# Kernel optimization log

Hardware: AMD Instinct MI355X
Metric: run time of the kernel (lower is better)

Reference implementation:

```python
import jax, jax.numpy as jnp
import numpy as np

CELL = 8
POS_MARGIN = 1.0
NEG_MARGIN = 0.2
LAMBDA_D = 250.0
LAMBDA_LOSS = 0.0001


def _resize_bilinear(x, out_h, out_w):
    # torch F.interpolate(..., mode='bilinear', align_corners=False) half-pixel sampling
    B, H, W = x.shape
    def axis(n_in, n_out):
        src = (jnp.arange(n_out, dtype=jnp.float32) + 0.5) * (n_in / n_out) - 0.5
        src = jnp.clip(src, 0.0, n_in - 1.0)
        i0 = jnp.floor(src).astype(jnp.int32)
        i1 = jnp.minimum(i0 + 1, n_in - 1)
        w = src - i0.astype(jnp.float32)
        return i0, i1, w
    r0, r1, wr = axis(H, out_h)
    xr = x[:, r0, :] * (1.0 - wr)[None, :, None] + x[:, r1, :] * wr[None, :, None]
    c0, c1, wc = axis(W, out_w)
    return xr[:, :, c0] * (1.0 - wc)[None, None, :] + xr[:, :, c1] * wc[None, None, :]


def detector_loss(pred, heatmap, vm):
    eps = 1e-7
    pos_inds = (heatmap == 1.0).astype(pred.dtype)
    neg_inds = (heatmap < 1.0).astype(pred.dtype)
    neg_weights = (1.0 - heatmap) ** 4
    num_pos = pos_inds.sum()
    pos_loss = (jnp.log(pred + eps) * (1.0 - pred) ** 2 * pos_inds * vm).sum()
    neg_loss = (jnp.log(1.0 - pred + eps) * pred ** 2 * neg_weights * neg_inds * vm).sum()
    return jnp.where(num_pos == 0, -neg_loss, -(pos_loss + neg_loss) / jnp.maximum(num_pos, 1.0))


def descriptor_loss(desc, wdesc, Hmat, vm, wvm):
    B, D, Hc, Wc = desc.shape
    N = Hc * Wc
    # cell-center coordinates in (row=y, col=x) order
    ii, jj = np.meshgrid(np.arange(Hc), np.arange(Wc), indexing='ij')
    coords = (np.stack([ii, jj], axis=-1) * CELL + CELL // 2).astype(np.float32)  # [Hc,Wc,2]
    coords = jnp.asarray(coords)
    pts = coords.reshape(-1, 2)
    # warp points with homographies (convert (y,x) -> (x,y), apply H, convert back)
    H_list = Hmat[:, 0]  # [B,3,3]
    homog = jnp.concatenate([pts[:, ::-1], jnp.ones((N, 1), jnp.float32)], axis=-1)  # [N,3]
    w = jnp.einsum('bij,nj->bni', H_list, homog)
    warped = (w[..., :2] / w[..., 2:3])[..., ::-1]  # back to (y,x), [B,N,2]
    warped = warped.reshape(B, Hc, Wc, 1, 1, 2)
    cell_dist = jnp.linalg.norm(coords.reshape(1, 1, 1, Hc, Wc, 2) - warped, axis=-1)  # [B,Hc,Wc,Hc,Wc]
    s = (cell_dist <= CELL - 0.5).astype(jnp.float32)

    normalization = wvm.sum()
    vm_c = _resize_bilinear(vm, Hc, Wc) > 0.5
    wvm_c = _resize_bilinear(wvm, Hc, Wc) > 0.5
    valid_pair = (vm_c.reshape(B, Hc, Wc, 1, 1) & wvm_c.reshape(B, 1, 1, Hc, Wc)).astype(jnp.float32)

    def l2norm(x):
        return x / jnp.maximum(jnp.linalg.norm(x, axis=-1, keepdims=True), 1e-12)

    d = l2norm(jnp.transpose(desc, (0, 2, 3, 1)))    # [B,Hc,Wc,D]
    wd = l2norm(jnp.transpose(wdesc, (0, 2, 3, 1)))  # [B,Hc,Wc,D]
    dot = jnp.einsum('bijd,bkld->bijkl', d, wd)      # all-pairs cosine sim
    dot = jax.nn.relu(dot)
    positive_dist = jnp.maximum(0.0, POS_MARGIN - dot)
    negative_dist = jnp.maximum(0.0, dot - NEG_MARGIN)
    loss = (LAMBDA_D * s * positive_dist + (1.0 - s) * negative_dist) * valid_pair
    return loss.sum() / normalization


def setup_inputs() -> dict:
    key = jax.random.key(0)
    ks = jax.random.split(key, 8)
    B, H, W, D, Hc, Wc = 2, 480, 640, 256, 60, 80
    Hmat = jnp.eye(3, dtype=jnp.float32)[None, None] + 0.05 * jax.random.normal(ks[6], (B, 1, 3, 3), jnp.float32)
    return {
        'prob': jax.random.uniform(ks[0], (B, H, W), jnp.float32),
        'ht': jax.random.uniform(ks[1], (B, H, W), jnp.float32),
        'valid_mask': jnp.ones((B, H, W), jnp.float32),
        'warped_prob': jax.random.uniform(ks[2], (B, H, W), jnp.float32),
        'warped_ht': jax.random.uniform(ks[3], (B, H, W), jnp.float32),
        'warped_valid_mask': jnp.ones((B, H, W), jnp.float32),
        'desc_raw': jax.random.normal(ks[4], (B, D, Hc, Wc), jnp.float32),
        'warped_desc_raw': jax.random.normal(ks[5], (B, D, Hc, Wc), jnp.float32),
        'Hmat': Hmat,
    }


def reference(prob, ht, valid_mask, warped_prob, warped_ht, warped_valid_mask, desc_raw, warped_desc_raw, Hmat):
    points_loss = detector_loss(prob, ht, valid_mask)
    warped_points_loss = detector_loss(warped_prob, warped_ht, warped_valid_mask)
    desc_loss = descriptor_loss(desc_raw, warped_desc_raw, Hmat, valid_mask, warped_valid_mask)
    total = points_loss + warped_points_loss + LAMBDA_LOSS * desc_loss
    return total, points_loss, warped_points_loss, desc_loss
```

## Files before the change

### kernel.cpp

```cpp
#include <hip/hip_runtime.h>
#include <hip/hip_bf16.h>
#include <cmath>

#define BB 2
#define HH 480
#define WW 640
#define DD 256
#define HC 60
#define WC 80
#define NN (HC*WC)

#define DET_BLOCKS 300
#define SUMSQ_NB ((NN + 255)/256)
#define P0_BLOCKS (2*DET_BLOCKS + 16*SUMSQ_NB)

#define NTILES64 (NN/64)
#define DESC_BLOCKS_F32 (BB*NTILES64*NTILES64)
#define TS3 96
#define BK 32
#define NT96 (NN/TS3)
#define BLK96 (NT96*NT96)
#define GEMM_BLOCKS (BB*BLK96)
#define CORR_BLOCKS (BB*NN/4)
#define DESC_GRID (GEMM_BLOCKS + CORR_BLOCKS)

#define OFF_DET0  0
#define OFF_DET1  2048
#define OFF_INVA  16384
#define OFF_INVB  (OFF_INVA + BB*NN)
#define OFF_WRW   (OFF_INVB + BB*NN)
#define OFF_WCL   (OFF_WRW + BB*NN)
#define OFF_VMC   (OFF_WCL + BB*NN)
#define OFF_WVMC  (OFF_VMC + BB*NN)
#define OFF_SQP   (OFF_WVMC + BB*NN)
#define OFF_DESCP (OFF_SQP + 16*NN)
#define OFF_TA    172032
#define TA_FLOATS (BB*NN*DD/2)
#define OFF_TB    (OFF_TA + TA_FLOATS)
#define WS_NEED   ((size_t)(OFF_TB + TA_FLOATS) * 4)

typedef __attribute__((ext_vector_type(8))) short short8;
typedef __attribute__((ext_vector_type(4))) float f32x4;

__device__ inline float bf2f(unsigned short u)
{
    unsigned int x = ((unsigned int)u) << 16;
    return __builtin_bit_cast(float, x);
}

__device__ inline void det_accum(float p, float h, float v,
                                 float& posl, float& negl, float& npos, float& vsum)
{
    float omp = 1.f - p;
    if (h == 1.0f) {
        posl += logf(p + 1e-7f) * omp*omp * v;
        npos += 1.f;
    }
    if (h < 1.0f) {
        float oh = 1.f - h;
        float w4 = oh*oh; w4 *= w4;
        negl += logf(omp + 1e-7f) * p*p * w4 * v;
    }
    vsum += v;
}

__global__ __launch_bounds__(256) void det_sumsq_kernel(
    const float* __restrict__ pred0, const float* __restrict__ hmap0, const float* __restrict__ vm0,
    const float* __restrict__ pred1, const float* __restrict__ hmap1, const float* __restrict__ vm1,
    const float* __restrict__ desc, const float* __restrict__ wdesc,
    float* __restrict__ ws)
{
    const int bidx = blockIdx.x;
    if (bidx >= 2*DET_BLOCKS) {
        const int sid   = bidx - 2*DET_BLOCKS;
        const int combo = sid / SUMSQ_NB;
        const int nb    = sid % SUMSQ_NB;
        const int z  = combo >> 2;
        const int dc = combo & 3;
        const int n  = nb*256 + threadIdx.x;
        if (n >= NN) return;
        const float* src = ((z & 1) ? wdesc : desc) + (size_t)(z >> 1)*DD*NN;
        float s = 0.f;
        const int d0 = dc*64;
        #pragma unroll 8
        for (int d = d0; d < d0 + 64; ++d) {
            float v = src[(size_t)d*NN + n];
            s = fmaf(v, v, s);
        }
        ws[OFF_SQP + ((size_t)z*4 + dc)*NN + n] = s;
        return;
    }
    const int set = bidx / DET_BLOCKS;
    const int db  = bidx % DET_BLOCKS;
    const float4* pred = (const float4*)(set ? pred1 : pred0);
    const float4* hmap = (const float4*)(set ? hmap1 : hmap0);
    const float4* vm   = (const float4*)(set ? vm1   : vm0);
    float* partials = ws + (set ? OFF_DET1 : OFF_DET0);

    float posl = 0.f, negl = 0.f, npos = 0.f, vsum = 0.f;
    const int total4 = BB*HH*WW/4;
    for (int i = db*256 + threadIdx.x; i < total4; i += DET_BLOCKS*256) {
        float4 p = pred[i], h = hmap[i], v = vm[i];
        det_accum(p.x, h.x, v.x, posl, negl, npos, vsum);
        det_accum(p.y, h.y, v.y, posl, negl, npos, vsum);
        det_accum(p.z, h.z, v.z, posl, negl, npos, vsum);
        det_accum(p.w, h.w, v.w, posl, negl, npos, vsum);
    }
    __shared__ float red[256];
    int t = threadIdx.x;
    float vals[4] = {posl, negl, npos, vsum};
    for (int j = 0; j < 4; ++j) {
        red[t] = vals[j]; __syncthreads();
        for (int s = 128; s > 0; s >>= 1) { if (t < s) red[t] += red[t+s]; __syncthreads(); }
        if (t == 0) partials[db*4 + j] = red[0];
        __syncthreads();
    }
}

__device__ inline float bilin_cell(const float* __restrict__ x, int i, int j)
{
    float sr = (i + 0.5f) * ((float)HH/(float)HC) - 0.5f;
    sr = fminf(fmaxf(sr, 0.f), (float)(HH-1));
    int r0 = (int)floorf(sr); int r1 = min(r0+1, HH-1); float wr = sr - (float)r0;
    float sc = (j + 0.5f) * ((float)WW/(float)WC) - 0.5f;
    sc = fminf(fmaxf(sc, 0.f), (float)(WW-1));
    int c0 = (int)floorf(sc); int c1 = min(c0+1, WW-1); float wc = sc - (float)c0;
    float v00 = x[r0*WW+c0], v01 = x[r0*WW+c1];
    float v10 = x[r1*WW+c0], v11 = x[r1*WW+c1];
    float e0 = v00*(1.f-wr) + v10*wr;
    float e1 = v01*(1.f-wr) + v11*wr;
    return e0*(1.f-wc) + e1*wc;
}

__device__ inline void prep_geom(int idx, const float* __restrict__ vm,
                                 const float* __restrict__ wvm,
                                 const float* __restrict__ Hmat, float* __restrict__ ws)
{
    int b = idx / NN, n = idx % NN;
    int i = n / WC, j = n % WC;
    float px = (float)(j*8 + 4), py = (float)(i*8 + 4);
    const float* Hb = Hmat + b*9;
    float w0 = Hb[0]*px + Hb[1]*py + Hb[2];
    float w1 = Hb[3]*px + Hb[4]*py + Hb[5];
    float w2 = Hb[6]*px + Hb[7]*py + Hb[8];
    ws[OFF_WRW + idx] = w1 / w2;
    ws[OFF_WCL + idx] = w0 / w2;
    ws[OFF_VMC  + idx] = (bilin_cell(vm  + (size_t)b*HH*WW, i, j) > 0.5f) ? 1.f : 0.f;
    ws[OFF_WVMC + idx] = (bilin_cell(wvm + (size_t)b*HH*WW, i, j) > 0.5f) ? 1.f : 0.f;
}

__global__ __launch_bounds__(256) void prep_kernel(
    const float* __restrict__ vm, const float* __restrict__ wvm,
    const float* __restrict__ Hmat, float* __restrict__ ws)
{
    int idx = blockIdx.x*256 + threadIdx.x;
    if (idx >= BB*NN) return;
    int b = idx / NN, n = idx % NN;

    const float* sq = ws + OFF_SQP;
    float sa = 0.f, sb = 0.f;
    #pragma unroll
    for (int k = 0; k < 4; ++k) {
        sa += sq[((b*2+0)*4 + k)*NN + n];
        sb += sq[((b*2+1)*4 + k)*NN + n];
    }
    ws[OFF_INVA + idx] = 1.f / fmaxf(sqrtf(sa), 1e-12f);
    ws[OFF_INVB + idx] = 1.f / fmaxf(sqrtf(sb), 1e-12f);
    prep_geom(idx, vm, wvm, Hmat, ws);
}

__global__ __launch_bounds__(256) void prep_kernel_full(
    const float* __restrict__ desc, const float* __restrict__ wdesc,
    const float* __restrict__ vm, const float* __restrict__ wvm,
    const float* __restrict__ Hmat, float* __restrict__ ws)
{
    int idx = blockIdx.x*256 + threadIdx.x;
    if (idx >= BB*NN) return;
    int b = idx / NN, n = idx % NN;

    const float* a  = desc  + (size_t)b*DD*NN + n;
    const float* bp = wdesc + (size_t)b*DD*NN + n;
    float sa = 0.f, sb = 0.f;
    for (int d = 0; d < DD; ++d) {
        float x = a[(size_t)d*NN];  sa = fmaf(x, x, sa);
        float y = bp[(size_t)d*NN]; sb = fmaf(y, y, sb);
    }
    ws[OFF_INVA + idx] = 1.f / fmaxf(sqrtf(sa), 1e-12f);
    ws[OFF_INVB + idx] = 1.f / fmaxf(sqrtf(sb), 1e-12f);
    prep_geom(idx, vm, wvm, Hmat, ws);
}

__global__ __launch_bounds__(256) void transpose_kernel(
    const float* __restrict__ desc, const float* __restrict__ wdesc,
    unsigned short* __restrict__ ta, unsigned short* __restrict__ tb,
    const float* __restrict__ ws)
{
    const int nb = blockIdx.x * 64;
    const int db = blockIdx.y * 64;
    const int z  = blockIdx.z;
    const int b  = z >> 1;
    const float* src = (z & 1) ? wdesc : desc;
    unsigned short* dst = (z & 1) ? tb : ta;
    src += (size_t)b*DD*NN;
    dst += (size_t)b*NN*DD;

    __shared__ float tile[64][65];
    const int tr = threadIdx.x >> 6;
    const int tc = threadIdx.x & 63;
    #pragma unroll
    for (int i = 0; i < 16; ++i) {
        int d = db + i*4 + tr;
        tile[i*4 + tr][tc] = src[(size_t)d*NN + nb + tc];
    }
    __syncthreads();
    const int idxn = b*NN + nb + tc;
    const float scl = (z & 1) ? ws[OFF_INVB + idxn] * ws[OFF_WVMC + idxn]
                              : ws[OFF_INVA + idxn] * ws[OFF_VMC  + idxn];
    #pragma unroll
    for (int gg = 0; gg < 2; ++gg) {
        int g = tr + gg*4;
        short8 v8;
        #pragma unroll
        for (int j = 0; j < 8; ++j) {
            float v = tile[g*8 + j][tc] * scl;
            __hip_bfloat16 h = __float2bfloat16(v);
            v8[j] = (short)__builtin_bit_cast(unsigned short, h);
        }
        int sg = (db >> 3) + g;
        *(short8*)(dst + ((size_t)sg*NN + nb + tc)*8) = v8;
    }
}

__global__ __launch_bounds__(256) void desc_mfma(
    const unsigned short* __restrict__ ta, const unsigned short* __restrict__ tb,
    const float* __restrict__ ws, float* __restrict__ partials)
{
    __shared__ unsigned short As[3][TS3*BK];
    __shared__ unsigned short Bs[3][TS3*BK];
    __shared__ float corr_red[4];

    const int bidx = blockIdx.x;
    const int tid  = threadIdx.x;
    const int lane = tid & 63;
    const int wid  = tid >> 6;

    if (bidx < CORR_BLOCKS) {
        const int idx = bidx*4 + wid;
        const int cb  = idx / NN, cn = idx % NN;
        const float wrow = ws[OFF_WRW + idx];
        const float wcol = ws[OFF_WCL + idx];
        const float va   = ws[OFF_VMC + idx];
        const unsigned short* tA = ta + (size_t)cb*NN*DD;
        const unsigned short* tB = tb + (size_t)cb*NN*DD;
        const float* wvmc = ws + OFF_WVMC + cb*NN;

        const int sg = lane >> 1;
        const int e  = (lane & 1) * 4;
        const unsigned short* ap = tA + ((size_t)sg*NN + cn)*8 + e;
        float a0 = bf2f(ap[0]), a1 = bf2f(ap[1]), a2 = bf2f(ap[2]), a3 = bf2f(ap[3]);

        const int ibase = (int)floorf((wrow - 4.f) * 0.125f);
        const int jbase = (int)floorf((wcol - 4.f) * 0.125f);
        float corr = 0.f;
        #pragma unroll
        for (int di = 0; di < 2; ++di) {
            #pragma unroll
            for (int dj = 0; dj < 2; ++dj) {
                int ii = ibase + di, jj = jbase + dj;
                float dr = (float)(ii*8 + 4) - wrow;
                float dc = (float)(jj*8 + 4) - wcol;
                bool ok = (ii >= 0) && (ii < HC) && (jj >= 0) && (jj < WC)
                          && (dr*dr + dc*dc) <= 56.25f;
                if (ok) {
                    int m = ii*WC + jj;
                    const unsigned short* bp = tB + ((size_t)sg*NN + m)*8 + e;
                    float d = a0*bf2f(bp[0]);
                    d = fmaf(a1, bf2f(bp[1]), d);
                    d = fmaf(a2, bf2f(bp[2]), d);
                    d = fmaf(a3, bf2f(bp[3]), d);
                    #pragma unroll
                    for (int off = 1; off < 64; off <<= 1)
                        d += __shfl_xor(d, off, 64);
                    float dotr = fmaxf(d, 0.f);
                    float pos = 250.f * fmaxf(1.f - dotr, 0.f);
                    float neg = fmaxf(d - 0.2f, 0.f);
                    corr += (pos - neg) * va * wvmc[m];
                }
            }
        }
        if (lane == 0) corr_red[wid] = corr;
        __syncthreads();
        if (tid == 0)
            partials[bidx] = corr_red[0] + corr_red[1] + corr_red[2] + corr_red[3];
        return;
    }

    const int g   = bidx - CORR_BLOCKS;
    const int swz = (g & 7) * (GEMM_BLOCKS/8) + (g >> 3);
    const int b   = swz / BLK96;
    const int rr  = swz % BLK96;
    const int n0  = (rr / NT96) * TS3;
    const int m0  = (rr % NT96) * TS3;

    const unsigned short* tab = ta + (size_t)b*NN*DD;
    const unsigned short* tbb = tb + (size_t)b*NN*DD;

#define STAGE(t_, buf_)                                                          \
    {                                                                            \
        _Pragma("unroll")                                                        \
        for (int c = 0; c < 3; ++c) {                                            \
            int c2 = wid*3 + c;                                                  \
            int cA = (c2 < 6) ? c2 : (c2 - 6);                                   \
            int o  = cA*64 + lane;                                               \
            int s  = o / TS3;                                                    \
            int r  = o - s*TS3;                                                  \
            const unsigned short* gp = (c2 < 6)                                  \
                ? (tab + ((size_t)((t_)*4 + s)*NN + n0 + r)*8)                   \
                : (tbb + ((size_t)((t_)*4 + s)*NN + m0 + r)*8);                  \
            unsigned short* l0 = (c2 < 6) ? &As[buf_][cA*512] : &Bs[buf_][cA*512];\
            __builtin_amdgcn_global_load_lds(                                    \
                (const __attribute__((address_space(1))) void*)gp,               \
                (__attribute__((address_space(3))) void*)l0, 16, 0, 0);          \
        }                                                                        \
    }

    const int wr = wid >> 1, wc = wid & 1;
    const int ln15   = lane & 15;
    const int slot16 = lane >> 4;
    f32x4 acc[3][3] = {};

    STAGE(0, 0);
    STAGE(1, 1);

    #pragma unroll
    for (int t = 0; t < 8; ++t) {
        if (t < 7) asm volatile("s_waitcnt vmcnt(3)" ::: "memory");
        else       asm volatile("s_waitcnt vmcnt(0)" ::: "memory");
        __builtin_amdgcn_s_barrier();
        __builtin_amdgcn_sched_barrier(0);
        const unsigned short* Ab = As[t % 3];
        const unsigned short* Bb = Bs[t % 3];
        short8 af[3], bf[3];
        #pragma unroll
        for (int f = 0; f < 3; ++f) {
            int ra = wr*48 + f*16 + ln15;
            af[f] = *(const short8*)(Ab + (slot16*TS3 + ra)*8);
            int rb = wc*48 + f*16 + ln15;
            bf[f] = *(const short8*)(Bb + (slot16*TS3 + rb)*8);
        }
        if (t < 6) STAGE(t+2, (t+2) % 3);
        #pragma unroll
        for (int fi = 0; fi < 3; ++fi)
            #pragma unroll
            for (int fj = 0; fj < 3; ++fj)
                acc[fi][fj] = __builtin_amdgcn_mfma_f32_16x16x32_bf16(
                    af[fi], bf[fj], acc[fi][fj], 0, 0, 0);
    }

    float sum = 0.f;
    #pragma unroll
    for (int fi = 0; fi < 3; ++fi)
        #pragma unroll
        for (int fj = 0; fj < 3; ++fj)
            #pragma unroll
            for (int reg = 0; reg < 4; ++reg)
                sum += fmaxf(acc[fi][fj][reg] - 0.2f, 0.f);

    float* red = (float*)&As[0][0];
    red[tid] = sum; __syncthreads();
    for (int s = 128; s > 0; s >>= 1) { if (tid < s) red[tid] += red[tid+s]; __syncthreads(); }
    if (tid == 0) partials[bidx] = red[0];
#undef STAGE
}

__global__ __launch_bounds__(256) void desc_kernel(
    const float* __restrict__ desc, const float* __restrict__ wdesc,
    const float* __restrict__ ws, float* __restrict__ partials)
{
    const int b  = blockIdx.z;
    const int n0 = blockIdx.y * 64;
    const int m0 = blockIdx.x * 64;
    const float* A  = desc  + (size_t)b*DD*NN;
    const float* Bm = wdesc + (size_t)b*DD*NN;

    __shared__ float As[32][64];
    __shared__ float Bs[32][64];

    const int tid = threadIdx.x;
    const int tx = tid & 15, ty = tid >> 4;
    float acc[4][4] = {{0.f}};

    for (int k0 = 0; k0 < DD; k0 += 32) {
        #pragma unroll
        for (int l = 0; l < 8; ++l) {
            int e = tid + l*256;
            int kk = e >> 6, nn = e & 63;
            As[kk][nn] = A [(size_t)(k0+kk)*NN + n0 + nn];
            Bs[kk][nn] = Bm[(size_t)(k0+kk)*NN + m0 + nn];
        }
        __syncthreads();
        #pragma unroll
        for (int kk = 0; kk < 32; ++kk) {
            float4 av = *reinterpret_cast<const float4*>(&As[kk][ty*4]);
            float4 bv = *reinterpret_cast<const float4*>(&Bs[kk][tx*4]);
            float a4[4] = {av.x, av.y, av.z, av.w};
            float b4[4] = {bv.x, bv.y, bv.z, bv.w};
            #pragma unroll
            for (int r = 0; r < 4; ++r)
                #pragma unroll
                for (int c = 0; c < 4; ++c)
                    acc[r][c] = fmaf(a4[r], b4[c], acc[r][c]);
        }
        __syncthreads();
    }

    const float* inva = ws + OFF_INVA + b*NN;
    const float* invb = ws + OFF_INVB + b*NN;
    const float* wrp  = ws + OFF_WRW + b*NN;
    const float* wcp  = ws + OFF_WCL + b*NN;
    const float* vmc  = ws + OFF_VMC + b*NN;
    const float* wvmc = ws + OFF_WVMC + b*NN;

    int nb = n0 + ty*4, mb = m0 + tx*4;
    float ia[4], wrv[4], wcv[4], va[4];
    #pragma unroll
    for (int r = 0; r < 4; ++r) {
        int n = nb + r;
        ia[r] = inva[n]; wrv[r] = wrp[n]; wcv[r] = wcp[n]; va[r] = vmc[n];
    }
    float ib[4], vb[4], crow[4], ccol[4];
    #pragma unroll
    for (int c = 0; c < 4; ++c) {
        int m = mb + c;
        ib[c] = invb[m]; vb[c] = wvmc[m];
        crow[c] = (float)((m / WC)*8 + 4);
        ccol[c] = (float)((m % WC)*8 + 4);
    }
    float sum = 0.f;
    #pragma unroll
    for (int r = 0; r < 4; ++r) {
        #pragma unroll
        for (int c = 0; c < 4; ++c) {
            float dot = fmaxf(acc[r][c] * ia[r] * ib[c], 0.f);
            float dr = crow[c] - wrv[r];
            float dc = ccol[c] - wcv[r];
            bool s = (dr*dr + dc*dc) <= 56.25f;
            float term = s ? 250.f * fmaxf(1.f - dot, 0.f)
                           : fmaxf(dot - 0.2f, 0.f);
            sum += term * va[r] * vb[c];
        }
    }

    __shared__ float red[256];
    red[tid] = sum; __syncthreads();
    for (int s = 128; s > 0; s >>= 1) { if (tid < s) red[tid] += red[tid+s]; __syncthreads(); }
    if (tid == 0) {
        int bid = (blockIdx.z * gridDim.y + blockIdx.y) * gridDim.x + blockIdx.x;
        partials[bid] = red[0];
    }
}

__global__ __launch_bounds__(256) void finalize_kernel(
    const float* __restrict__ ws, float* __restrict__ out, int desc_nblocks)
{
    __shared__ float red[256];
    int t = threadIdx.x;
    float res[2];
    float norm = 0.f;
    for (int pass = 0; pass < 2; ++pass) {
        const float* p = ws + (pass == 0 ? OFF_DET0 : OFF_DET1);
        float s0=0.f, s1=0.f, s2=0.f, s3=0.f;
        for (int i = t; i < DET_BLOCKS; i += 256) {
            s0 += p[i*4+0]; s1 += p[i*4+1]; s2 += p[i*4+2]; s3 += p[i*4+3];
        }
        float v[4] = {s0,s1,s2,s3};
        float tot[4];
        for (int j = 0; j < 4; ++j) {
            red[t] = v[j]; __syncthreads();
            for (int s = 128; s > 0; s >>= 1) { if (t < s) red[t] += red[t+s]; __syncthreads(); }
            tot[j] = red[0]; __syncthreads();
        }
        float posl = tot[0], negl = tot[1], npos = tot[2], vsum = tot[3];
        res[pass] = (npos == 0.f) ? -negl : -(posl + negl) / fmaxf(npos, 1.f);
        if (pass == 1) norm = vsum;
    }
    float ds = 0.f;
    for (int i = t; i < desc_nblocks; i += 256) ds += ws[OFF_DESCP + i];
    red[t] = ds; __syncthreads();
    for (int s = 128; s > 0; s >>= 1) { if (t < s) red[t] += red[t+s]; __syncthreads(); }
    float descsum = red[0];
    if (t == 0) {
        float desc_loss = descsum / norm;
        float total = res[0] + res[1] + 1e-4f * desc_loss;
        out[0] = total;
        out[1] = res[0];
        out[2] = res[1];
        out[3] = desc_loss;
    }
}

extern "C" void kernel_launch(void* const* d_in, const int* in_sizes, int n_in,
                              void* d_out, int out_size, void* d_ws, size_t ws_size,
                              hipStream_t stream)
{
    const float* prob  = (const float*)d_in[0];
    const float* htm   = (const float*)d_in[1];
    const float* vmask = (const float*)d_in[2];
    const float* wprob = (const float*)d_in[3];
    const float* wht   = (const float*)d_in[4];
    const float* wvm   = (const float*)d_in[5];
    const float* desc  = (const float*)d_in[6];
    const float* wdesc = (const float*)d_in[7];
    const float* Hm    = (const float*)d_in[8];
    float* ws  = (float*)d_ws;
    float* out = (float*)d_out;

    if (ws_size >= WS_NEED) {
        unsigned short* ta = (unsigned short*)(ws + OFF_TA);
        unsigned short* tb = (unsigned short*)(ws + OFF_TB);
        det_sumsq_kernel<<<P0_BLOCKS, 256, 0, stream>>>(
            prob, htm, vmask, wprob, wht, wvm, desc, wdesc, ws);
        prep_kernel<<<(BB*NN + 255)/256, 256, 0, stream>>>(vmask, wvm, Hm, ws);
        transpose_kernel<<<dim3(NN/64, DD/64, BB*2), 256, 0, stream>>>(desc, wdesc, ta, tb, ws);
        desc_mfma<<<DESC_GRID, 256, 0, stream>>>(ta, tb, ws, ws + OFF_DESCP);
        finalize_kernel<<<1, 256, 0, stream>>>(ws, out, DESC_GRID);
    } else {
        det_sumsq_kernel<<<2*DET_BLOCKS, 256, 0, stream>>>(
            prob, htm, vmask, wprob, wht, wvm, desc, wdesc, ws);
        prep_kernel_full<<<(BB*NN + 255)/256, 256, 0, stream>>>(desc, wdesc, vmask, wvm, Hm, ws);
        desc_kernel<<<dim3(NTILES64, NTILES64, BB), 256, 0, stream>>>(desc, wdesc, ws, ws + OFF_DESCP);
        finalize_kernel<<<1, 256, 0, stream>>>(ws, out, DESC_BLOCKS_F32);
    }
}
```

Baseline: 67.53 us.

## Restructure kernel schedule: merge prep into phase1, move detector loss into GEMM launch

Folds the geometry prep into the sum-of-squares kernel, which removes one launch. The inverse-norm computation moves into the transpose kernel, which reads the partial sums of squares directly. The detector-loss reduction moves out of the first kernel and runs as extra blocks appended to the MFMA descriptor grid, so that memory-bound work can overlap with the compute-bound GEMM tail. The cost is that the GEMM launch gets heavier, with 600 extra blocks that may compete for CUs and reuse the As shared buffer for the reduction.

```diff
diff --git a/kernel.cpp b/kernel.cpp
--- a/kernel.cpp
+++ b/kernel.cpp
@@ -12,7 +12,8 @@
 
 #define DET_BLOCKS 300
 #define SUMSQ_NB ((NN + 255)/256)
-#define P0_BLOCKS (2*DET_BLOCKS + 16*SUMSQ_NB)
+#define GEOM_NB ((BB*NN + 255)/256)
+#define P1_BLOCKS (16*SUMSQ_NB + GEOM_NB)
 
 #define NTILES64 (NN/64)
 #define DESC_BLOCKS_F32 (BB*NTILES64*NTILES64)
@@ -22,7 +23,9 @@
 #define BLK96 (NT96*NT96)
 #define GEMM_BLOCKS (BB*BLK96)
 #define CORR_BLOCKS (BB*NN/4)
-#define DESC_GRID (GEMM_BLOCKS + CORR_BLOCKS)
+#define DET_ROLE_BLOCKS (2*DET_BLOCKS)
+#define DESC_PARTIALS (GEMM_BLOCKS + CORR_BLOCKS)
+#define DESC_GRID (DESC_PARTIALS + DET_ROLE_BLOCKS)
 
 #define OFF_DET0  0
 #define OFF_DET1  2048
@@ -64,17 +67,76 @@
     vsum += v;
 }
 
-__global__ __launch_bounds__(256) void det_sumsq_kernel(
+__device__ inline void det_role(
+    int set, int db, int tid,
     const float* __restrict__ pred0, const float* __restrict__ hmap0, const float* __restrict__ vm0,
     const float* __restrict__ pred1, const float* __restrict__ hmap1, const float* __restrict__ vm1,
+    float* __restrict__ ws, float* __restrict__ red)
+{
+    const float4* pred = (const float4*)(set ? pred1 : pred0);
+    const float4* hmap = (const float4*)(set ? hmap1 : hmap0);
+    const float4* vm   = (const float4*)(set ? vm1   : vm0);
+    float* partials = ws + (set ? OFF_DET1 : OFF_DET0);
+
+    float posl = 0.f, negl = 0.f, npos = 0.f, vsum = 0.f;
+    const int total4 = BB*HH*WW/4;
+    for (int i = db*256 + tid; i < total4; i += DET_BLOCKS*256) {
+        float4 p = pred[i], h = hmap[i], v = vm[i];
+        det_accum(p.x, h.x, v.x, posl, negl, npos, vsum);
+        det_accum(p.y, h.y, v.y, posl, negl, npos, vsum);
+        det_accum(p.z, h.z, v.z, posl, negl, npos, vsum);
+        det_accum(p.w, h.w, v.w, posl, negl, npos, vsum);
+    }
+    float vals[4] = {posl, negl, npos, vsum};
+    for (int j = 0; j < 4; ++j) {
+        red[tid] = vals[j]; __syncthreads();
+        for (int s = 128; s > 0; s >>= 1) { if (tid < s) red[tid] += red[tid+s]; __syncthreads(); }
+        if (tid == 0) partials[db*4 + j] = red[0];
+        __syncthreads();
+    }
+}
+
+__device__ inline float bilin_cell(const float* __restrict__ x, int i, int j)
+{
+    float sr = (i + 0.5f) * ((float)HH/(float)HC) - 0.5f;
+    sr = fminf(fmaxf(sr, 0.f), (float)(HH-1));
+    int r0 = (int)floorf(sr); int r1 = min(r0+1, HH-1); float wr = sr - (float)r0;
+    float sc = (j + 0.5f) * ((float)WW/(float)WC) - 0.5f;
+    sc = fminf(fmaxf(sc, 0.f), (float)(WW-1));
+    int c0 = (int)floorf(sc); int c1 = min(c0+1, WW-1); float wc = sc - (float)c0;
+    float v00 = x[r0*WW+c0], v01 = x[r0*WW+c1];
+    float v10 = x[r1*WW+c0], v11 = x[r1*WW+c1];
+    float e0 = v00*(1.f-wr) + v10*wr;
+    float e1 = v01*(1.f-wr) + v11*wr;
+    return e0*(1.f-wc) + e1*wc;
+}
+
+__device__ inline void prep_geom(int idx, const float* __restrict__ vm,
+                                 const float* __restrict__ wvm,
+                                 const float* __restrict__ Hmat, float* __restrict__ ws)
+{
+    int b = idx / NN, n = idx % NN;
+    int i = n / WC, j = n % WC;
+    float px = (float)(j*8 + 4), py = (float)(i*8 + 4);
+    const float* Hb = Hmat + b*9;
+    float w0 = Hb[0]*px + Hb[1]*py + Hb[2];
+    float w1 = Hb[3]*px + Hb[4]*py + Hb[5];
+    float w2 = Hb[6]*px + Hb[7]*py + Hb[8];
+    ws[OFF_WRW + idx] = w1 / w2;
+    ws[OFF_WCL + idx] = w0 / w2;
+    ws[OFF_VMC  + idx] = (bilin_cell(vm  + (size_t)b*HH*WW, i, j) > 0.5f) ? 1.f : 0.f;
+    ws[OFF_WVMC + idx] = (bilin_cell(wvm + (size_t)b*HH*WW, i, j) > 0.5f) ? 1.f : 0.f;
+}
+
+__global__ __launch_bounds__(256) void phase1_kernel(
     const float* __restrict__ desc, const float* __restrict__ wdesc,
-    float* __restrict__ ws)
+    const float* __restrict__ vm, const float* __restrict__ wvm,
+    const float* __restrict__ Hmat, float* __restrict__ ws)
 {
     const int bidx = blockIdx.x;
-    if (bidx >= 2*DET_BLOCKS) {
-        const int sid   = bidx - 2*DET_BLOCKS;
-        const int combo = sid / SUMSQ_NB;
-        const int nb    = sid % SUMSQ_NB;
+    if (bidx < 16*SUMSQ_NB) {
+        const int combo = bidx / SUMSQ_NB;
+        const int nb    = bidx % SUMSQ_NB;
         const int z  = combo >> 2;
         const int dc = combo & 3;
         const int n  = nb*256 + threadIdx.x;
@@ -90,82 +152,8 @@
         ws[OFF_SQP + ((size_t)z*4 + dc)*NN + n] = s;
         return;
     }
-    const int set = bidx / DET_BLOCKS;
-    const int db  = bidx % DET_BLOCKS;
-    const float4* pred = (const float4*)(set ? pred1 : pred0);
-    const float4* hmap = (const float4*)(set ? hmap1 : hmap0);
-    const float4* vm   = (const float4*)(set ? vm1   : vm0);
-    float* partials = ws + (set ? OFF_DET1 : OFF_DET0);
-
-    float posl = 0.f, negl = 0.f, npos = 0.f, vsum = 0.f;
-    const int total4 = BB*HH*WW/4;
-    for (int i = db*256 + threadIdx.x; i < total4; i += DET_BLOCKS*256) {
-        float4 p = pred[i], h = hmap[i], v = vm[i];
-        det_accum(p.x, h.x, v.x, posl, negl, npos, vsum);
-        det_accum(p.y, h.y, v.y, posl, negl, npos, vsum);
-        det_accum(p.z, h.z, v.z, posl, negl, npos, vsum);
-        det_accum(p.w, h.w, v.w, posl, negl, npos, vsum);
-    }
-    __shared__ float red[256];
-    int t = threadIdx.x;
-    float vals[4] = {posl, negl, npos, vsum};
-    for (int j = 0; j < 4; ++j) {
-        red[t] = vals[j]; __syncthreads();
-        for (int s = 128; s > 0; s >>= 1) { if (t < s) red[t] += red[t+s]; __syncthreads(); }
-        if (t == 0) partials[db*4 + j] = red[0];
-        __syncthreads();
-    }
-}
-
-__device__ inline float bilin_cell(const float* __restrict__ x, int i, int j)
-{
-    float sr = (i + 0.5f) * ((float)HH/(float)HC) - 0.5f;
-    sr = fminf(fmaxf(sr, 0.f), (float)(HH-1));
-    int r0 = (int)floorf(sr); int r1 = min(r0+1, HH-1); float wr = sr - (float)r0;
-    float sc = (j + 0.5f) * ((float)WW/(float)WC) - 0.5f;
-    sc = fminf(fmaxf(sc, 0.f), (float)(WW-1));
-    int c0 = (int)floorf(sc); int c1 = min(c0+1, WW-1); float wc = sc - (float)c0;
-    float v00 = x[r0*WW+c0], v01 = x[r0*WW+c1];
-    float v10 = x[r1*WW+c0], v11 = x[r1*WW+c1];
-    float e0 = v00*(1.f-wr) + v10*wr;
-    float e1 = v01*(1.f-wr) + v11*wr;
-    return e0*(1.f-wc) + e1*wc;
-}
-
-__device__ inline void prep_geom(int idx, const float* __restrict__ vm,
-                                 const float* __restrict__ wvm,
-                                 const float* __restrict__ Hmat, float* __restrict__ ws)
-{
-    int b = idx / NN, n = idx % NN;
-    int i = n / WC, j = n % WC;
-    float px = (float)(j*8 + 4), py = (float)(i*8 + 4);
-    const float* Hb = Hmat + b*9;
-    float w0 = Hb[0]*px + Hb[1]*py + Hb[2];
-    float w1 = Hb[3]*px + Hb[4]*py + Hb[5];
-    float w2 = Hb[6]*px + Hb[7]*py + Hb[8];
-    ws[OFF_WRW + idx] = w1 / w2;
-    ws[OFF_WCL + idx] = w0 / w2;
-    ws[OFF_VMC  + idx] = (bilin_cell(vm  + (size_t)b*HH*WW, i, j) > 0.5f) ? 1.f : 0.f;
-    ws[OFF_WVMC + idx] = (bilin_cell(wvm + (size_t)b*HH*WW, i, j) > 0.5f) ? 1.f : 0.f;
-}
-
-__global__ __launch_bounds__(256) void prep_kernel(
-    const float* __restrict__ vm, const float* __restrict__ wvm,
-    const float* __restrict__ Hmat, float* __restrict__ ws)
-{
-    int idx = blockIdx.x*256 + threadIdx.x;
+    const int idx = (bidx - 16*SUMSQ_NB)*256 + threadIdx.x;
     if (idx >= BB*NN) return;
-    int b = idx / NN, n = idx % NN;
-
-    const float* sq = ws + OFF_SQP;
-    float sa = 0.f, sb = 0.f;
-    #pragma unroll
-    for (int k = 0; k < 4; ++k) {
-        sa += sq[((b*2+0)*4 + k)*NN + n];
-        sb += sq[((b*2+1)*4 + k)*NN + n];
-    }
-    ws[OFF_INVA + idx] = 1.f / fmaxf(sqrtf(sa), 1e-12f);
-    ws[OFF_INVB + idx] = 1.f / fmaxf(sqrtf(sb), 1e-12f);
     prep_geom(idx, vm, wvm, Hmat, ws);
 }
 
@@ -188,6 +176,16 @@
     ws[OFF_INVA + idx] = 1.f / fmaxf(sqrtf(sa), 1e-12f);
     ws[OFF_INVB + idx] = 1.f / fmaxf(sqrtf(sb), 1e-12f);
     prep_geom(idx, vm, wvm, Hmat, ws);
+}
+
+__global__ __launch_bounds__(256) void det_kernel(
+    const float* __restrict__ pred0, const float* __restrict__ hmap0, const float* __restrict__ vm0,
+    const float* __restrict__ pred1, const float* __restrict__ hmap1, const float* __restrict__ vm1,
+    float* __restrict__ ws)
+{
+    __shared__ float red[256];
+    det_role(blockIdx.x / DET_BLOCKS, blockIdx.x % DET_BLOCKS, threadIdx.x,
+             pred0, hmap0, vm0, pred1, hmap1, vm1, ws, red);
 }
 
 __global__ __launch_bounds__(256) void transpose_kernel(
@@ -213,9 +211,15 @@
         tile[i*4 + tr][tc] = src[(size_t)d*NN + nb + tc];
     }
     __syncthreads();
-    const int idxn = b*NN + nb + tc;
-    const float scl = (z & 1) ? ws[OFF_INVB + idxn] * ws[OFF_WVMC + idxn]
-                              : ws[OFF_INVA + idxn] * ws[OFF_VMC  + idxn];
+    const int n = nb + tc;
+    const int gidx = b*NN + n;
+    float ss = 0.f;
+    #pragma unroll
+    for (int k = 0; k < 4; ++k)
+        ss += ws[OFF_SQP + ((size_t)z*4 + k)*NN + n];
+    const float inv  = 1.f / fmaxf(sqrtf(ss), 1e-12f);
+    const float mask = (z & 1) ? ws[OFF_WVMC + gidx] : ws[OFF_VMC + gidx];
+    const float scl  = inv * mask;
     #pragma unroll
     for (int gg = 0; gg < 2; ++gg) {
         int g = tr + gg*4;
@@ -233,6 +237,8 @@
 
 __global__ __launch_bounds__(256) void desc_mfma(
     const unsigned short* __restrict__ ta, const unsigned short* __restrict__ tb,
+    const float* __restrict__ pred0, const float* __restrict__ hmap0, const float* __restrict__ vm0,
+    const float* __restrict__ pred1, const float* __restrict__ hmap1, const float* __restrict__ vm1,
     const float* __restrict__ ws, float* __restrict__ partials)
 {
     __shared__ unsigned short As[3][TS3*BK];
@@ -244,8 +250,18 @@
     const int lane = tid & 63;
     const int wid  = tid >> 6;
 
-    if (bidx < CORR_BLOCKS) {
-        const int idx = bidx*4 + wid;
+    if (bidx >= GEMM_BLOCKS + CORR_BLOCKS) {
+        const int did = bidx - GEMM_BLOCKS - CORR_BLOCKS;
+        float* red = (float*)&As[0][0];
+        det_role(did / DET_BLOCKS, did % DET_BLOCKS, tid,
+                 pred0, hmap0, vm0, pred1, hmap1, vm1,
+                 (float*)ws, red);
+        return;
+    }
+
+    if (bidx >= GEMM_BLOCKS) {
+        const int cid = bidx - GEMM_BLOCKS;
+        const int idx = cid*4 + wid;
         const int cb  = idx / NN, cn = idx % NN;
         const float wrow = ws[OFF_WRW + idx];
         const float wcol = ws[OFF_WCL + idx];
@@ -295,7 +311,7 @@
         return;
     }
 
-    const int g   = bidx - CORR_BLOCKS;
+    const int g   = bidx;
     const int swz = (g & 7) * (GEMM_BLOCKS/8) + (g >> 3);
     const int b   = swz / BLK96;
     const int rr  = swz % BLK96;
@@ -518,15 +534,14 @@
     if (ws_size >= WS_NEED) {
         unsigned short* ta = (unsigned short*)(ws + OFF_TA);
         unsigned short* tb = (unsigned short*)(ws + OFF_TB);
-        det_sumsq_kernel<<<P0_BLOCKS, 256, 0, stream>>>(
-            prob, htm, vmask, wprob, wht, wvm, desc, wdesc, ws);
-        prep_kernel<<<(BB*NN + 255)/256, 256, 0, stream>>>(vmask, wvm, Hm, ws);
+        phase1_kernel<<<P1_BLOCKS, 256, 0, stream>>>(desc, wdesc, vmask, wvm, Hm, ws);
         transpose_kernel<<<dim3(NN/64, DD/64, BB*2), 256, 0, stream>>>(desc, wdesc, ta, tb, ws);
-        desc_mfma<<<DESC_GRID, 256, 0, stream>>>(ta, tb, ws, ws + OFF_DESCP);
-        finalize_kernel<<<1, 256, 0, stream>>>(ws, out, DESC_GRID);
+        desc_mfma<<<DESC_GRID, 256, 0, stream>>>(
+            ta, tb, prob, htm, vmask, wprob, wht, wvm, ws, ws + OFF_DESCP);
+        finalize_kernel<<<1, 256, 0, stream>>>(ws, out, DESC_PARTIALS);
     } else {
-        det_sumsq_kernel<<<2*DET_BLOCKS, 256, 0, stream>>>(
-            prob, htm, vmask, wprob, wht, wvm, desc, wdesc, ws);
+        det_kernel<<<2*DET_BLOCKS, 256, 0, stream>>>(
+            prob, htm, vmask, wprob, wht, wvm, ws);
         prep_kernel_full<<<(BB*NN + 255)/256, 256, 0, stream>>>(desc, wdesc, vmask, wvm, Hm, ws);
         desc_kernel<<<dim3(NTILES64, NTILES64, BB), 256, 0, stream>>>(desc, wdesc, ws, ws + OFF_DESCP);
         finalize_kernel<<<1, 256, 0, stream>>>(ws, out, DESC_BLOCKS_F32);
```

New measurement: 66.26 us. About the same (-1.9%).
